# Kernel tuning notes

Measured on AMD Instinct MI355X. Metric: run time of the kernel, lower is better.

The kernel has to match this reference:

```python
import jax, jax.numpy as jnp
import numpy as np

KSIZE = 3
SOFTMAX_SCALE = 10.0


def extract_patches(x):
    # x: [B, C, H, W] -> patches [B, H*W, C, 3, 3]
    # Matches F.unfold(same_padding(x), kernel=3, stride=1) then
    # reshape(B, C, 3, 3, L).permute(0, 4, 1, 2, 3).
    B, C, H, W = x.shape
    xp = jnp.pad(x, ((0, 0), (0, 0), (1, 1), (1, 1)))
    # p[b, c, i, j, y, x] = xp[b, c, y+i, x+j]
    p = jnp.stack(
        [jnp.stack([xp[:, :, i:i + H, j:j + W] for j in range(KSIZE)], axis=2)
         for i in range(KSIZE)], axis=2)  # [B, C, 3, 3, H, W]
    return p.transpose(0, 4, 5, 1, 2, 3).reshape(B, H * W, C, KSIZE, KSIZE)


def _conv_same(x, w):
    # x: [Cin, H, W], w: [Cout, Cin, 3, 3] -> [Cout, H, W] (pad 1, stride 1)
    return jax.lax.conv_general_dilated(
        x[None], w, window_strides=(1, 1), padding=((1, 1), (1, 1)),
        dimension_numbers=('NCHW', 'OIHW', 'NCHW'))[0]


def setup_inputs() -> dict:
    key = jax.random.key(0)
    kf, kb = jax.random.split(key)
    f = jax.random.normal(kf, (4, 64, 64, 64), dtype=jnp.float32)
    b = jax.random.normal(kb, (4, 64, 64, 64), dtype=jnp.float32)
    return {"f": f, "b": b}


def reference(f, b):
    B, C, Hf, Wf = f.shape
    # Per-sample dynamic kernels from background patches: [B, L, C, 3, 3]
    w = extract_patches(b)
    # Correlation: per-sample conv of f with its own L patch-kernels -> [B, L, Hf, Wf]
    scores = jax.vmap(_conv_same)(f, w)
    # Scaled softmax over the L patch axis
    attn = jax.nn.softmax(scores * SOFTMAX_SCALE, axis=1)
    # conv_transpose2d(attn, w, stride=1, padding=1) == SAME conv with
    # spatially-flipped kernels and in/out channels swapped.
    w_t = jnp.flip(w, axis=(-2, -1)).transpose(0, 2, 1, 3, 4)  # [B, C, L, 3, 3]
    y = jax.vmap(_conv_same)(attn, w_t) / 9.0  # [B, C, Hf, Wf]
    return (y, w.reshape(B, -1, KSIZE, KSIZE))
```

## Files before the change

### kernel.cpp

```cpp
#include <hip/hip_runtime.h>
#include <hip/hip_bf16.h>
#include <hip/hip_fp16.h>
#include <stdint.h>


typedef unsigned short ushort_t;
typedef __attribute__((ext_vector_type(8))) short bf16x8;
typedef __attribute__((ext_vector_type(4))) float f32x4;

__device__ __forceinline__ float bf2f(ushort_t u){
  union { float f; uint32_t i; } v; v.i = ((uint32_t)u) << 16; return v.f;
}
__device__ __forceinline__ ushort_t f2bf(float f){
  union { float f; uint32_t i; } v; v.f = f;
  uint32_t x = v.i;
  return (ushort_t)((x + 0x7fffu + ((x >> 16) & 1u)) >> 16);
}

__global__ __launch_bounds__(256) void k_prep(const float* __restrict__ bin,
                                              float* __restrict__ wout,
                                              float* __restrict__ yzero){
  int t = blockIdx.x * 256 + threadIdx.x;
  yzero[t] = 0.f;
  int c  = t & 63;
  int l  = (t >> 6) & 4095;
  int bb = t >> 18;
  int y = l >> 6, x = l & 63;
  const float* src = bin + (((size_t)(bb * 64 + c)) << 12);
  float* dst = wout + (size_t)t * 9;
  #pragma unroll
  for (int i = 0; i < 3; i++){
    int yy = y + i - 1;
    #pragma unroll
    for (int j = 0; j < 3; j++){
      int xx = x + j - 1;
      float v = 0.f;
      if ((unsigned)yy < 64u && (unsigned)xx < 64u) v = src[(yy << 6) + xx];
      dst[i * 3 + j] = v;
    }
  }
}

__global__ __launch_bounds__(256, 2) void k_rgemm(const float* __restrict__ f,
                                                  const float* __restrict__ bin,
                                                  float* __restrict__ R,
                                                  int bt0){
  __shared__ float As[64][128];
  __shared__ float Bs[64][128];
  int bt = bt0 + blockIdx.z;
  int m0 = blockIdx.x << 7;
  int n0 = blockIdx.y << 7;
  const float* fb = f   + (((size_t)bt) << 18);
  const float* bb = bin + (((size_t)bt) << 18);
  int t = threadIdx.x;
  for (int idx = t; idx < 64 * 128; idx += 256){
    int c = idx >> 7, m = idx & 127;
    As[c][m] = fb[(c << 12) + m0 + m];
    Bs[c][m] = bb[(c << 12) + n0 + m];
  }
  __syncthreads();
  int tx = t & 15, ty = t >> 4;
  float acc[8][8];
  #pragma unroll
  for (int i = 0; i < 8; i++)
    #pragma unroll
    for (int j = 0; j < 8; j++) acc[i][j] = 0.f;

  for (int c = 0; c < 64; c++){
    float4 a0 = *(const float4*)&As[c][(ty << 3)];
    float4 a1 = *(const float4*)&As[c][(ty << 3) + 4];
    float4 b0 = *(const float4*)&Bs[c][(tx << 2)];
    float4 b1 = *(const float4*)&Bs[c][64 + (tx << 2)];
    float av[8] = {a0.x, a0.y, a0.z, a0.w, a1.x, a1.y, a1.z, a1.w};
    float bv[8] = {b0.x, b0.y, b0.z, b0.w, b1.x, b1.y, b1.z, b1.w};
    #pragma unroll
    for (int i = 0; i < 8; i++)
      #pragma unroll
      for (int j = 0; j < 8; j++) acc[i][j] += av[i] * bv[j];
  }
  #pragma unroll
  for (int i = 0; i < 8; i++){
    float* dst = R + ((size_t)(m0 + (ty << 3) + i) << 12) + n0;
    *(float4*)(dst + (tx << 2))      = make_float4(acc[i][0], acc[i][1], acc[i][2], acc[i][3]);
    *(float4*)(dst + 64 + (tx << 2)) = make_float4(acc[i][4], acc[i][5], acc[i][6], acc[i][7]);
  }
}

__global__ __launch_bounds__(256, 2) void k_softmax4(const float* __restrict__ R,
                                                     ushort_t* __restrict__ attn,
                                                     float* __restrict__ scale){
  __shared__ float Rt[24][648];
  const int t  = threadIdx.x;
  const int bb = blockIdx.x;
  const int inner = bb >> 3;
  const int ty = ((bb & 7) << 1) | (inner & 1);
  const int tx = inner >> 1;
  const int p0 = ty << 2, q0 = tx << 1;
  const int qi = t >> 5, kt = t & 31;
  const int pi = qi >> 1, qj = qi & 1;
  const int ktx = kt & 15;

  float M = -3.0e38f, L = 0.f;
  float mref[8];
  float4 rbuf[16];

  int row = ((p0 + pi) << 6) + q0 + qj;
  ushort_t* arow = attn + ((size_t)row << 12);

  #pragma unroll
  for (int i = 0; i < 16; i++){
    int idx = t + (i << 8);
    float4 v = make_float4(0.f, 0.f, 0.f, 0.f);
    if (idx < 3888){
      unsigned r = (unsigned)idx / 162u;
      int fo = idx - (int)r * 162;
      int rp = p0 - 1 + (int)(r >> 2);
      int rq = q0 - 1 + (int)(r & 3);
      int kg = -68 + (fo << 2);
      if ((unsigned)rp < 64u && (unsigned)rq < 64u && (unsigned)kg <= 4092u)
        v = *(const float4*)(R + (((size_t)((rp << 6) + rq)) << 12) + kg);
    }
    rbuf[i] = v;
  }

  #pragma unroll
  for (int c = 0; c < 8; c++){
    __syncthreads();
    #pragma unroll
    for (int i = 0; i < 16; i++){
      int idx = t + (i << 8);
      if (idx < 3888) ((float4*)&Rt[0][0])[idx] = rbuf[i];
    }
    __syncthreads();
    if (c < 7){
      const int k0 = (c + 1) << 9;
      #pragma unroll
      for (int i = 0; i < 16; i++){
        int idx = t + (i << 8);
        float4 v = make_float4(0.f, 0.f, 0.f, 0.f);
        if (idx < 3888){
          unsigned r = (unsigned)idx / 162u;
          int fo = idx - (int)r * 162;
          int rp = p0 - 1 + (int)(r >> 2);
          int rq = q0 - 1 + (int)(r & 3);
          int kg = k0 - 68 + (fo << 2);
          if ((unsigned)rp < 64u && (unsigned)rq < 64u && (unsigned)kg <= 4092u)
            v = *(const float4*)(R + (((size_t)((rp << 6) + rq)) << 12) + kg);
        }
        rbuf[i] = v;
      }
    }
    float4 sv[4];
    #pragma unroll
    for (int j = 0; j < 4; j++){
      int y = (c << 3) + (j << 1) + (kt >> 4);
      int sa0 = (j << 7) + (kt << 2) + 68;
      float4 s = make_float4(0.f, 0.f, 0.f, 0.f);
      #pragma unroll
      for (int a = -1; a <= 1; a++){
        if ((unsigned)(y + a) < 64u){
          int rb = (pi + 1 + a) << 2;
          int sa = sa0 + (a << 6);
          float4 A0 = *(const float4*)&Rt[rb + qj][sa];
          float4 A1 = *(const float4*)&Rt[rb + qj + 1][sa];
          float4 A2 = *(const float4*)&Rt[rb + qj + 2][sa];
          float Lv = __shfl_up(A0.w, 1);
          float Rv = __shfl_down(A2.x, 1);
          s.x += (ktx == 0 ? 0.f : Lv) + A1.x + A2.y;
          s.y += A0.x + A1.y + A2.z;
          s.z += A0.y + A1.z + A2.w;
          s.w += A0.z + A1.w + (ktx == 15 ? 0.f : Rv);
        }
      }
      s.x *= 10.f; s.y *= 10.f; s.z *= 10.f; s.w *= 10.f;
      sv[j] = s;
    }
    float mc = M;
    #pragma unroll
    for (int j = 0; j < 4; j++)
      mc = fmaxf(mc, fmaxf(fmaxf(sv[j].x, sv[j].y), fmaxf(sv[j].z, sv[j].w)));
    #pragma unroll
    for (int off = 1; off < 32; off <<= 1) mc = fmaxf(mc, __shfl_xor(mc, off));
    float lnew = L * __expf(M - mc);
    #pragma unroll
    for (int j = 0; j < 4; j++){
      float ex = __expf(sv[j].x - mc), ey = __expf(sv[j].y - mc);
      float ez = __expf(sv[j].z - mc), ew = __expf(sv[j].w - mc);
      lnew += ex + ey + ez + ew;
      ushort4 o; o.x = f2bf(ex); o.y = f2bf(ey); o.z = f2bf(ez); o.w = f2bf(ew);
      *(ushort4*)&arow[(c << 9) + (j << 7) + (kt << 2)] = o;
    }
    L = lnew; M = mc; mref[c] = mc;
  }
  #pragma unroll
  for (int off = 1; off < 32; off <<= 1) L += __shfl_xor(L, off);
  if (kt == 0){
    float invL = 1.0f / L;
    float4 s0, s1;
    s0.x = __expf(mref[0] - M) * invL; s0.y = __expf(mref[1] - M) * invL;
    s0.z = __expf(mref[2] - M) * invL; s0.w = __expf(mref[3] - M) * invL;
    s1.x = __expf(mref[4] - M) * invL; s1.y = __expf(mref[5] - M) * invL;
    s1.z = __expf(mref[6] - M) * invL; s1.w = __expf(mref[7] - M) * invL;
    *(float4*)&scale[(row << 3)]     = s0;
    *(float4*)&scale[(row << 3) + 4] = s1;
  }
}

__global__ __launch_bounds__(256, 2) void k_pstencil5(const ushort_t* __restrict__ attn,
                                                      const float* __restrict__ scale,
                                                      ushort_t* __restrict__ P){
  __shared__ float At[24][648];
  __shared__ float Sc[24][8];
  const int t  = threadIdx.x;
  const int bb = blockIdx.x;
  const int inner = bb >> 3;
  const int ty = ((bb & 7) << 1) | (inner & 1);
  const int tx = inner >> 1;
  const int p0 = ty << 2, q0 = tx << 1;
  const int qi = t >> 5, kt = t & 31;
  const int pi = qi >> 1, qj = qi & 1;
  const int ktx = kt & 15;

  int row = ((p0 + pi) << 6) + q0 + qj;
  ushort_t* prow = P + ((size_t)row << 12);
  const float inv9 = 1.0f / 9.0f;

  if (t < 192){
    int r = t >> 3, cc = t & 7;
    int rp = p0 - 1 + (r >> 2);
    int rq = q0 - 1 + (r & 3);
    float v = 0.f;
    if ((unsigned)rp < 64u && (unsigned)rq < 64u)
      v = scale[(((rp << 6) + rq) << 3) + cc];
    Sc[r][cc] = v;
  }

  uint2 rbuf[16];
  #pragma unroll
  for (int i = 0; i < 16; i++){
    int idx = t + (i << 8);
    uint2 v = make_uint2(0u, 0u);
    if (idx < 3888){
      unsigned r = (unsigned)idx / 162u;
      int fo = idx - (int)r * 162;
      int rp = p0 - 1 + (int)(r >> 2);
      int rq = q0 - 1 + (int)(r & 3);
      int kg = -68 + (fo << 2);
      if ((unsigned)rp < 64u && (unsigned)rq < 64u && (unsigned)kg <= 4092u)
        v = *(const uint2*)(attn + (((size_t)((rp << 6) + rq)) << 12) + kg);
    }
    rbuf[i] = v;
  }

  #pragma unroll
  for (int c = 0; c < 8; c++){
    __syncthreads();
    #pragma unroll
    for (int i = 0; i < 16; i++){
      int idx = t + (i << 8);
      if (idx < 3888){
        unsigned r = (unsigned)idx / 162u;
        int fo = idx - (int)r * 162;
        int key = (c << 9) - 68 + (fo << 2);
        key = key < 0 ? 0 : (key > 4095 ? 4095 : key);
        float sc = Sc[r][key >> 9];
        uint2 u = rbuf[i];
        float4 w;
        { union { uint32_t q; float f; } a_, b_;
          a_.q = u.x << 16; b_.q = u.x & 0xffff0000u; w.x = a_.f * sc; w.y = b_.f * sc; }
        { union { uint32_t q; float f; } a_, b_;
          a_.q = u.y << 16; b_.q = u.y & 0xffff0000u; w.z = a_.f * sc; w.w = b_.f * sc; }
        ((float4*)&At[0][0])[idx] = w;
      }
    }
    __syncthreads();
    if (c < 7){
      const int k0 = (c + 1) << 9;
      #pragma unroll
      for (int i = 0; i < 16; i++){
        int idx = t + (i << 8);
        uint2 v = make_uint2(0u, 0u);
        if (idx < 3888){
          unsigned r = (unsigned)idx / 162u;
          int fo = idx - (int)r * 162;
          int rp = p0 - 1 + (int)(r >> 2);
          int rq = q0 - 1 + (int)(r & 3);
          int kg = k0 - 68 + (fo << 2);
          if ((unsigned)rp < 64u && (unsigned)rq < 64u && (unsigned)kg <= 4092u)
            v = *(const uint2*)(attn + (((size_t)((rp << 6) + rq)) << 12) + kg);
        }
        rbuf[i] = v;
      }
    }
    #pragma unroll
    for (int j = 0; j < 4; j++){
      int y = (c << 3) + (j << 1) + (kt >> 4);
      int sa0 = (j << 7) + (kt << 2) + 68;
      float4 s = make_float4(0.f, 0.f, 0.f, 0.f);
      #pragma unroll
      for (int a = -1; a <= 1; a++){
        if ((unsigned)(y + a) < 64u){
          int rb = (pi + 1 + a) << 2;
          int sa = sa0 + (a << 6);
          float4 A0 = *(const float4*)&At[rb + qj][sa];
          float4 A1 = *(const float4*)&At[rb + qj + 1][sa];
          float4 A2 = *(const float4*)&At[rb + qj + 2][sa];
          float Lv = __shfl_up(A0.w, 1);
          float Rv = __shfl_down(A2.x, 1);
          s.x += (ktx == 0 ? 0.f : Lv) + A1.x + A2.y;
          s.y += A0.x + A1.y + A2.z;
          s.z += A0.y + A1.z + A2.w;
          s.w += A0.z + A1.w + (ktx == 15 ? 0.f : Rv);
        }
      }
      ushort4 o;
      o.x = f2bf(s.x * inv9);
      o.y = f2bf(s.y * inv9);
      o.z = f2bf(s.z * inv9);
      o.w = f2bf(s.w * inv9);
      *(ushort4*)&prow[(c << 9) + (j << 7) + (kt << 2)] = o;
    }
  }
}

__global__ __launch_bounds__(256) void k_ygemm2(const float* __restrict__ bin,
                                                const ushort_t* __restrict__ P,
                                                float* __restrict__ y,
                                                int bt){
  const int t = threadIdx.x;
  const int lane = t & 63, wv = t >> 6;
  const int n = lane & 15, quad = lane >> 4;
  const int pq0 = blockIdx.x << 6;
  const int k0  = blockIdx.y << 8;
  const float*    bbase = bin + (((size_t)bt) << 18);
  const ushort_t* Prow  = P + (((size_t)(pq0 + (wv << 4) + n)) << 12);

  f32x4 acc[4];
  #pragma unroll
  for (int cb = 0; cb < 4; cb++) acc[cb] = (f32x4){0.f, 0.f, 0.f, 0.f};

  #pragma unroll 2
  for (int kb = k0; kb < k0 + 256; kb += 32){
    int ko = kb + (quad << 3);
    bf16x8 pf = *(const bf16x8*)(Prow + ko);
    #pragma unroll
    for (int cb = 0; cb < 4; cb++){
      const float* bp = bbase + (((cb << 4) + n) << 12) + ko;
      float4 b0 = *(const float4*)bp;
      float4 b1 = *(const float4*)(bp + 4);
      bf16x8 bf;
      bf[0] = (short)f2bf(b0.x); bf[1] = (short)f2bf(b0.y);
      bf[2] = (short)f2bf(b0.z); bf[3] = (short)f2bf(b0.w);
      bf[4] = (short)f2bf(b1.x); bf[5] = (short)f2bf(b1.y);
      bf[6] = (short)f2bf(b1.z); bf[7] = (short)f2bf(b1.w);
      acc[cb] = __builtin_amdgcn_mfma_f32_16x16x32_bf16(bf, pf, acc[cb], 0, 0, 0);
    }
  }
  int pql = pq0 + (wv << 4) + n;
  #pragma unroll
  for (int cb = 0; cb < 4; cb++)
    #pragma unroll
    for (int r = 0; r < 4; r++){
      int c = (cb << 4) + (quad << 2) + r;
      atomicAdd(&y[(((size_t)(bt * 64 + c)) << 12) + pql], acc[cb][r]);
    }
}

extern "C" void kernel_launch(void* const* d_in, const int* in_sizes, int n_in,
                              void* d_out, int out_size, void* d_ws, size_t ws_size,
                              hipStream_t stream){
  const float* f = (const float*)d_in[0];
  const float* b = (const float*)d_in[1];
  float* out  = (float*)d_out;
  float* yout = out;
  float* wout = out + 1048576;

  const size_t RB  = 4096ull * 4096 * 4;
  const size_t AB  = 4096ull * 4096 * 2;

  k_prep<<<4096, 256, 0, stream>>>(b, wout, yout);

  float*    R     = (float*)d_ws;
  ushort_t* attn  = (ushort_t*)((char*)d_ws + RB);
  float*    scale = (float*)((char*)d_ws + RB + AB);
  ushort_t* P     = (ushort_t*)d_ws;
  for (int bt = 0; bt < 4; bt++){
    k_rgemm    <<<dim3(32, 32, 1), 256, 0, stream>>>(f, b, R, bt);
    k_softmax4 <<<512, 256, 0, stream>>>(R, attn, scale);
    k_pstencil5<<<512, 256, 0, stream>>>(attn, scale, P);
    k_ygemm2   <<<dim3(64, 16), 256, 0, stream>>>(b, P, yout, bt);
  }
}
```

Baseline: 663.0 us.

## Batch multiple samples per launch and stage patch output through LDS

The per-sample loop of four kernels now processes up to four samples per launch via a grid z/y dimension, with the workspace split into per-sample slices sized by the available ws_size. The intent is to fill the GPU with more blocks per launch and cut launch count and tail effects. The patch-extraction kernel also stages its 9-float outputs in shared memory so the global writes become coalesced float4 stores. The cost is a larger workspace footprint and more cache pressure when several samples run at once.

```diff
diff --git a/kernel.cpp b/kernel.cpp
--- a/kernel.cpp
+++ b/kernel.cpp
@@ -8,6 +8,11 @@
 typedef __attribute__((ext_vector_type(8))) short bf16x8;
 typedef __attribute__((ext_vector_type(4))) float f32x4;
 
+#define RSTRIDE  16777216ull
+#define ASTRIDE  16777216ull
+#define PSTRIDE  33554432ull
+#define SSTRIDE  32768ull
+
 __device__ __forceinline__ float bf2f(ushort_t u){
   union { float f; uint32_t i; } v; v.i = ((uint32_t)u) << 16; return v.f;
 }
@@ -17,17 +22,19 @@
   return (ushort_t)((x + 0x7fffu + ((x >> 16) & 1u)) >> 16);
 }
 
-__global__ __launch_bounds__(256) void k_prep(const float* __restrict__ bin,
-                                              float* __restrict__ wout,
-                                              float* __restrict__ yzero){
-  int t = blockIdx.x * 256 + threadIdx.x;
+__global__ __launch_bounds__(256) void k_prep2(const float* __restrict__ bin,
+                                               float* __restrict__ wout,
+                                               float* __restrict__ yzero){
+  __shared__ float ls[2304];
+  int tid = threadIdx.x;
+  int t = blockIdx.x * 256 + tid;
   yzero[t] = 0.f;
   int c  = t & 63;
   int l  = (t >> 6) & 4095;
   int bb = t >> 18;
   int y = l >> 6, x = l & 63;
   const float* src = bin + (((size_t)(bb * 64 + c)) << 12);
-  float* dst = wout + (size_t)t * 9;
+  float* dst = ls + tid * 9;
   #pragma unroll
   for (int i = 0; i < 3; i++){
     int yy = y + i - 1;
@@ -39,6 +46,11 @@
       dst[i * 3 + j] = v;
     }
   }
+  __syncthreads();
+  float* wbase = wout + (size_t)blockIdx.x * 2304;
+  #pragma unroll
+  for (int idx = tid; idx < 576; idx += 256)
+    *(float4*)(wbase + (idx << 2)) = *(const float4*)(ls + (idx << 2));
 }
 
 __global__ __launch_bounds__(256, 2) void k_rgemm(const float* __restrict__ f,
@@ -52,6 +64,7 @@
   int n0 = blockIdx.y << 7;
   const float* fb = f   + (((size_t)bt) << 18);
   const float* bb = bin + (((size_t)bt) << 18);
+  float* Rb = R + (size_t)blockIdx.z * RSTRIDE;
   int t = threadIdx.x;
   for (int idx = t; idx < 64 * 128; idx += 256){
     int c = idx >> 7, m = idx & 127;
@@ -80,18 +93,21 @@
   }
   #pragma unroll
   for (int i = 0; i < 8; i++){
-    float* dst = R + ((size_t)(m0 + (ty << 3) + i) << 12) + n0;
+    float* dst = Rb + ((size_t)(m0 + (ty << 3) + i) << 12) + n0;
     *(float4*)(dst + (tx << 2))      = make_float4(acc[i][0], acc[i][1], acc[i][2], acc[i][3]);
     *(float4*)(dst + 64 + (tx << 2)) = make_float4(acc[i][4], acc[i][5], acc[i][6], acc[i][7]);
   }
 }
 
-__global__ __launch_bounds__(256, 2) void k_softmax4(const float* __restrict__ R,
-                                                     ushort_t* __restrict__ attn,
-                                                     float* __restrict__ scale){
+__global__ __launch_bounds__(256, 2) void k_softmax4(const float* __restrict__ Rg,
+                                                     ushort_t* __restrict__ attng,
+                                                     float* __restrict__ scaleg){
   __shared__ float Rt[24][648];
   const int t  = threadIdx.x;
   const int bb = blockIdx.x;
+  const float* R = Rg + (size_t)blockIdx.y * RSTRIDE;
+  ushort_t* attn = attng + (size_t)blockIdx.y * ASTRIDE;
+  float* scale = scaleg + (size_t)blockIdx.y * SSTRIDE;
   const int inner = bb >> 3;
   const int ty = ((bb & 7) << 1) | (inner & 1);
   const int tx = inner >> 1;
@@ -206,13 +222,16 @@
   }
 }
 
-__global__ __launch_bounds__(256, 2) void k_pstencil5(const ushort_t* __restrict__ attn,
-                                                      const float* __restrict__ scale,
-                                                      ushort_t* __restrict__ P){
+__global__ __launch_bounds__(256, 2) void k_pstencil5(const ushort_t* __restrict__ attng,
+                                                      const float* __restrict__ scaleg,
+                                                      ushort_t* __restrict__ Pg){
   __shared__ float At[24][648];
   __shared__ float Sc[24][8];
   const int t  = threadIdx.x;
   const int bb = blockIdx.x;
+  const ushort_t* attn = attng + (size_t)blockIdx.y * ASTRIDE;
+  const float* scale = scaleg + (size_t)blockIdx.y * SSTRIDE;
+  ushort_t* P = Pg + (size_t)blockIdx.y * PSTRIDE;
   const int inner = bb >> 3;
   const int ty = ((bb & 7) << 1) | (inner & 1);
   const int tx = inner >> 1;
@@ -324,16 +343,18 @@
 }
 
 __global__ __launch_bounds__(256) void k_ygemm2(const float* __restrict__ bin,
-                                                const ushort_t* __restrict__ P,
+                                                const ushort_t* __restrict__ Pg,
                                                 float* __restrict__ y,
-                                                int bt){
+                                                int bt0){
   const int t = threadIdx.x;
   const int lane = t & 63, wv = t >> 6;
   const int n = lane & 15, quad = lane >> 4;
+  const int bt = bt0 + blockIdx.z;
   const int pq0 = blockIdx.x << 6;
   const int k0  = blockIdx.y << 8;
   const float*    bbase = bin + (((size_t)bt) << 18);
-  const ushort_t* Prow  = P + (((size_t)(pq0 + (wv << 4) + n)) << 12);
+  const ushort_t* Prow  = Pg + (size_t)blockIdx.z * PSTRIDE
+                             + (((size_t)(pq0 + (wv << 4) + n)) << 12);
 
   f32x4 acc[4];
   #pragma unroll
@@ -375,19 +396,25 @@
   float* yout = out;
   float* wout = out + 1048576;
 
-  const size_t RB  = 4096ull * 4096 * 4;
-  const size_t AB  = 4096ull * 4096 * 2;
-
-  k_prep<<<4096, 256, 0, stream>>>(b, wout, yout);
+  const size_t RB  = RSTRIDE * 4;
+  const size_t AB  = ASTRIDE * 2;
+  const size_t SCB = SSTRIDE * 4;
+  const size_t PER = RB + AB + SCB;
+
+  int nb = 1;
+  if (ws_size >= 4 * PER) nb = 4;
+  else if (ws_size >= 2 * PER) nb = 2;
+
+  k_prep2<<<4096, 256, 0, stream>>>(b, wout, yout);
 
   float*    R     = (float*)d_ws;
-  ushort_t* attn  = (ushort_t*)((char*)d_ws + RB);
-  float*    scale = (float*)((char*)d_ws + RB + AB);
+  ushort_t* attn  = (ushort_t*)((char*)d_ws + (size_t)nb * RB);
+  float*    scale = (float*)((char*)d_ws + (size_t)nb * (RB + AB));
   ushort_t* P     = (ushort_t*)d_ws;
-  for (int bt = 0; bt < 4; bt++){
-    k_rgemm    <<<dim3(32, 32, 1), 256, 0, stream>>>(f, b, R, bt);
-    k_softmax4 <<<512, 256, 0, stream>>>(R, attn, scale);
-    k_pstencil5<<<512, 256, 0, stream>>>(attn, scale, P);
-    k_ygemm2   <<<dim3(64, 16), 256, 0, stream>>>(b, P, yout, bt);
-  }
-}
+  for (int bt0 = 0; bt0 < 4; bt0 += nb){
+    k_rgemm    <<<dim3(32, 32, nb), 256, 0, stream>>>(f, b, R, bt0);
+    k_softmax4 <<<dim3(512, nb),    256, 0, stream>>>(R, attn, scale);
+    k_pstencil5<<<dim3(512, nb),    256, 0, stream>>>(attn, scale, P);
+    k_ygemm2   <<<dim3(64, 16, nb), 256, 0, stream>>>(b, P, yout, bt0);
+  }
+}
```

New measurement: 594.6 us. -10.3%, faster.
